# Optimization experiments

Measured on AMD Instinct MI355X. Metric: run time of the kernel, lower is better.

The kernel has to match this reference:

```python
import jax, jax.numpy as jnp
import numpy as np

N_GRAPHS = 64  # number of graphs pooled by global_mean_pool


def setup_inputs() -> dict:
    key = jax.random.key(0)
    ks = jax.random.split(key, 10)
    N, E, H, K = 50000, 800000, 128, 3
    x = jax.random.normal(ks[0], (N, H), dtype=jnp.float32)
    edge_index = jax.random.randint(ks[1], (2, E), 0, N)
    edge_weight = jax.random.uniform(ks[2], (E,), dtype=jnp.float32)
    batch = jnp.sort(jax.random.randint(ks[3], (N,), 0, N_GRAPHS))
    # 5 TAGConv layers, each with K+1 = 4 weight matrices [H,H] and one bias [H]
    conv_ws = jax.random.normal(ks[4], (5, K + 1, H, H), dtype=jnp.float32) * 0.05
    conv_bs = jax.random.normal(ks[5], (5, H), dtype=jnp.float32) * 0.01
    lin1_w = jax.random.normal(ks[6], (H, H), dtype=jnp.float32) * 0.05
    lin1_b = jnp.zeros((H,), dtype=jnp.float32)
    lin2_w = jax.random.normal(ks[7], (H, 1), dtype=jnp.float32) * 0.05
    lin2_b = jnp.zeros((1,), dtype=jnp.float32)
    return {"x": x, "edge_index": edge_index, "edge_weight": edge_weight,
            "batch": batch, "conv_ws": conv_ws, "conv_bs": conv_bs,
            "lin1_w": lin1_w, "lin1_b": lin1_b, "lin2_w": lin2_w, "lin2_b": lin2_b}


def _gcn_norm(edge_index, edge_weight, n):
    # TAGConv default: gcn_norm without self-loops
    row, col = edge_index[0], edge_index[1]
    deg = jax.ops.segment_sum(edge_weight, col, num_segments=n)
    deg_safe = jnp.where(deg > 0, deg, 1.0)
    dis = jnp.where(deg > 0, jax.lax.rsqrt(deg_safe), 0.0)
    return dis[row] * edge_weight * dis[col]


def _tagconv(x, w, b, row, col, norm, n):
    # out = sum_k (A_hat^k x) W_k + b
    out = x @ w[0]
    h = x
    for k in range(1, w.shape[0]):
        h = jax.ops.segment_sum(h[row] * norm[:, None], col, num_segments=n)
        out = out + h @ w[k]
    return out + b


def reference(x, edge_index, edge_weight, batch, conv_ws, conv_bs,
              lin1_w, lin1_b, lin2_w, lin2_b):
    n = x.shape[0]
    row, col = edge_index[0], edge_index[1]
    norm = _gcn_norm(edge_index, edge_weight, n)
    h = x
    for i in range(5):
        h = jax.nn.relu(_tagconv(h, conv_ws[i], conv_bs[i], row, col, norm, n))
    # global mean pool per graph (dropout treated as identity / eval mode)
    sums = jax.ops.segment_sum(h, batch, num_segments=N_GRAPHS)
    cnt = jax.ops.segment_sum(jnp.ones((n,), h.dtype), batch, num_segments=N_GRAPHS)
    g = sums / jnp.maximum(cnt, 1.0)[:, None]
    g = g @ lin1_w + lin1_b
    g = g @ lin2_w + lin2_b
    return jax.nn.sigmoid(g)
```

## Files before the change

kernel.cpp:

```cpp
#include <hip/hip_runtime.h>
#include <math.h>

#define H 128
#define NGRAPH 64

using f32x4 = __attribute__((ext_vector_type(4))) float;
using f32x2 = __attribute__((ext_vector_type(2))) float;

__device__ inline float bf2f(ushort u) {
  unsigned int b = ((unsigned int)u) << 16;
  return __builtin_bit_cast(float, b);
}
__device__ inline ushort f2bf(float f) {
  unsigned int u = __builtin_bit_cast(unsigned int, f);
  u = (u + 0x7FFF + ((u >> 16) & 1)) >> 16;
  return (ushort)u;
}

#define ACC8(accv, v, n)                                                                     \
  {                                                                                          \
    f32x2 c;                                                                                 \
    c = __builtin_amdgcn_cvt_pk_f32_fp8((v).x, false);                                       \
    accv[0] = fmaf(n, c[0], accv[0]); accv[1] = fmaf(n, c[1], accv[1]);                      \
    c = __builtin_amdgcn_cvt_pk_f32_fp8((v).x, true);                                        \
    accv[2] = fmaf(n, c[0], accv[2]); accv[3] = fmaf(n, c[1], accv[3]);                      \
    c = __builtin_amdgcn_cvt_pk_f32_fp8((v).y, false);                                       \
    accv[4] = fmaf(n, c[0], accv[4]); accv[5] = fmaf(n, c[1], accv[5]);                      \
    c = __builtin_amdgcn_cvt_pk_f32_fp8((v).y, true);                                        \
    accv[6] = fmaf(n, c[0], accv[6]); accv[7] = fmaf(n, c[1], accv[7]);                      \
  }

__global__ __launch_bounds__(256) void k_cvt_x(const float* __restrict__ x,
                                               unsigned char* __restrict__ x8, int total4) {
  int i = blockIdx.x * blockDim.x + threadIdx.x;
  if (i >= total4) return;
  float4 v = *(const float4*)(x + (size_t)i * 4);
  int p = __builtin_amdgcn_cvt_pk_fp8_f32(v.x, v.y, 0, false);
  p = __builtin_amdgcn_cvt_pk_fp8_f32(v.z, v.w, p, true);
  *(unsigned int*)(x8 + (size_t)i * 4) = (unsigned int)p;
}

__global__ __launch_bounds__(256) void k_cvt_w(const float* __restrict__ w,
                                               unsigned char* __restrict__ w8, int total4) {
  int i = blockIdx.x * blockDim.x + threadIdx.x;
  if (i >= total4) return;
  int f = i * 4;
  int l = f >> 16;
  int j = (f >> 9) & 127;
  int k = f & 511;
  int q = k >> 7, kk = k & 127;
  const float* src = w + (((size_t)(l * 4 + q) * H + kk) * H + j);
  float v0 = src[0], v1 = src[H], v2 = src[2 * H], v3 = src[3 * H];
  int p = __builtin_amdgcn_cvt_pk_fp8_f32(v0, v1, 0, false);
  p = __builtin_amdgcn_cvt_pk_fp8_f32(v2, v3, p, true);
  *(unsigned int*)(w8 + f) = (unsigned int)p;
}

__global__ void k_count(const int* __restrict__ col, int* __restrict__ cnt,
                        int* __restrict__ rank, int E) {
  int e = blockIdx.x * blockDim.x + threadIdx.x;
  if (e < E) rank[e] = atomicAdd(&cnt[col[e]], 1);
}

__global__ __launch_bounds__(256) void k_scan1(const int* __restrict__ cnt,
                                               int* __restrict__ bsum, int N) {
  int i = blockIdx.x * 256 + threadIdx.x;
  int v = (i < N) ? cnt[i] : 0;
  __shared__ int red[256];
  red[threadIdx.x] = v;
  __syncthreads();
  #pragma unroll
  for (int o = 128; o; o >>= 1) {
    if (threadIdx.x < o) red[threadIdx.x] += red[threadIdx.x + o];
    __syncthreads();
  }
  if (threadIdx.x == 0) bsum[blockIdx.x] = red[0];
}

__global__ __launch_bounds__(256) void k_scan2(const int* __restrict__ bsum,
                                               int* __restrict__ boff, int nb) {
  __shared__ int s[256];
  int t = threadIdx.x;
  int v = (t < nb) ? bsum[t] : 0;
  s[t] = v;
  __syncthreads();
  #pragma unroll
  for (int d = 1; d < 256; d <<= 1) {
    int u = (t >= d) ? s[t - d] : 0;
    __syncthreads();
    s[t] += u;
    __syncthreads();
  }
  if (t < nb) boff[t] = s[t] - v;
}

__global__ __launch_bounds__(256) void k_scan3(const int* __restrict__ cnt,
                                               const int* __restrict__ boff,
                                               int* __restrict__ ptr, int N) {
  int t = threadIdx.x;
  int i = blockIdx.x * 256 + t;
  int v = (i < N) ? cnt[i] : 0;
  __shared__ int s[256];
  s[t] = v;
  __syncthreads();
  #pragma unroll
  for (int d = 1; d < 256; d <<= 1) {
    int u = (t >= d) ? s[t - d] : 0;
    __syncthreads();
    s[t] += u;
    __syncthreads();
  }
  int ex = boff[blockIdx.x] + s[t] - v;
  if (i < N) {
    ptr[i] = ex;
    if (i == N - 1) ptr[N] = ex + v;
  }
}

__global__ void k_scatter(const int* __restrict__ row, const int* __restrict__ col,
                          const float* __restrict__ w, const int* __restrict__ ptr,
                          const int* __restrict__ rank, unsigned int* __restrict__ es, int E) {
  int e = blockIdx.x * blockDim.x + threadIdx.x;
  if (e < E) {
    int pos = ptr[col[e]] + rank[e];
    es[pos] = ((unsigned int)row[e] & 0xFFFFu) | ((unsigned int)f2bf(w[e]) << 16);
  }
}

__global__ __launch_bounds__(256) void k_degnorm1(const int* __restrict__ ptr,
                                                  const unsigned int* __restrict__ es,
                                                  float* __restrict__ dis, int N) {
  int v = blockIdx.x * blockDim.x + threadIdx.x;
  if (v >= N) return;
  int s = ptr[v], e = ptr[v + 1];
  float d = 0.f;
  for (int i = s; i < e; i++) d += bf2f((ushort)(es[i] >> 16));
  dis[v] = d > 0.f ? rsqrtf(d) : 0.f;
}

__global__ __launch_bounds__(256) void k_degnorm2(const int* __restrict__ ptr,
                                                  unsigned int* __restrict__ es,
                                                  const float* __restrict__ dis, int N) {
  int v = blockIdx.x * blockDim.x + threadIdx.x;
  if (v >= N) return;
  int s = ptr[v], e = ptr[v + 1];
  float dv = dis[v];
  for (int i = s; i < e; i++) {
    unsigned int u = es[i];
    float nm = dis[u & 0xFFFFu] * bf2f((ushort)(u >> 16)) * dv;
    es[i] = (u & 0xFFFFu) | ((unsigned int)f2bf(nm) << 16);
  }
}

__global__ __launch_bounds__(256) void k_prop(const unsigned char* __restrict__ hin8,
                                              unsigned char* __restrict__ hout8,
                                              const int* __restrict__ ptr,
                                              const unsigned int* __restrict__ es, int N) {
  int node = (blockIdx.x * 256 + threadIdx.x) >> 4;
  if (node >= N) return;
  int l15 = threadIdx.x & 15;
  int s = ptr[node], e = ptr[node + 1];
  float a[8] = {0.f, 0.f, 0.f, 0.f, 0.f, 0.f, 0.f, 0.f};
  float b[8] = {0.f, 0.f, 0.f, 0.f, 0.f, 0.f, 0.f, 0.f};
  const unsigned char* base = hin8 + l15 * 8;
  int i = s;
  for (; i + 3 < e; i += 4) {
    unsigned int u0 = es[i], u1 = es[i + 1], u2 = es[i + 2], u3 = es[i + 3];
    uint2 v0 = *(const uint2*)(base + (size_t)(u0 & 0xFFFFu) * H);
    uint2 v1 = *(const uint2*)(base + (size_t)(u1 & 0xFFFFu) * H);
    uint2 v2 = *(const uint2*)(base + (size_t)(u2 & 0xFFFFu) * H);
    uint2 v3 = *(const uint2*)(base + (size_t)(u3 & 0xFFFFu) * H);
    float n0 = bf2f((ushort)(u0 >> 16));
    float n1 = bf2f((ushort)(u1 >> 16));
    float n2 = bf2f((ushort)(u2 >> 16));
    float n3 = bf2f((ushort)(u3 >> 16));
    ACC8(a, v0, n0);
    ACC8(b, v1, n1);
    ACC8(a, v2, n2);
    ACC8(b, v3, n3);
  }
  for (; i < e; i++) {
    unsigned int u0 = es[i];
    uint2 v0 = *(const uint2*)(base + (size_t)(u0 & 0xFFFFu) * H);
    float n0 = bf2f((ushort)(u0 >> 16));
    ACC8(a, v0, n0);
  }
  #pragma unroll
  for (int j = 0; j < 8; j++) a[j] += b[j];
  int p0 = __builtin_amdgcn_cvt_pk_fp8_f32(a[0], a[1], 0, false);
  p0 = __builtin_amdgcn_cvt_pk_fp8_f32(a[2], a[3], p0, true);
  int p1 = __builtin_amdgcn_cvt_pk_fp8_f32(a[4], a[5], 0, false);
  p1 = __builtin_amdgcn_cvt_pk_fp8_f32(a[6], a[7], p1, true);
  *(uint2*)(hout8 + (size_t)node * H + l15 * 8) = make_uint2((unsigned int)p0, (unsigned int)p1);
}

__global__ __launch_bounds__(256) void k_fgemm(const unsigned char* __restrict__ X0,
                                               const unsigned char* __restrict__ X1,
                                               const unsigned char* __restrict__ X2,
                                               const unsigned char* __restrict__ X3,
                                               const unsigned char* __restrict__ W8,
                                               const float* __restrict__ bias,
                                               unsigned char* __restrict__ O8, int N) {
  __shared__ unsigned char As[128][72];
  __shared__ unsigned char Bs[128][72];
  int t = threadIdx.x;
  int r0 = blockIdx.x * 128;
  int w = t >> 6, lane = t & 63;
  int mw = w >> 1, nw = w & 1;
  int l15 = lane & 15, l4 = lane >> 4;

  f32x4 acc[4][4];
  #pragma unroll
  for (int i = 0; i < 4; i++)
    #pragma unroll
    for (int j = 0; j < 4; j++) acc[i][j] = (f32x4){0.f, 0.f, 0.f, 0.f};

  for (int it = 0; it < 8; ++it) {
    const unsigned char* Xp = (it < 2) ? X0 : (it < 4) ? X1 : (it < 6) ? X2 : X3;
    int kb = (it & 1) * 64;
    int k0 = it * 64;
    #pragma unroll
    for (int p = 0; p < 2; p++) {
      int idx = t + p * 256;
      int rj = idx >> 2;
      int kc = (idx & 3) << 4;
      int gr = r0 + rj;
      uint4 av = make_uint4(0, 0, 0, 0);
      if (gr < N) av = *(const uint4*)(Xp + (size_t)gr * H + kb + kc);
      *(uint4*)&As[rj][kc] = av;
      *(uint4*)&Bs[rj][kc] = *(const uint4*)(W8 + (size_t)rj * 512 + k0 + kc);
    }
    __syncthreads();
    #pragma unroll
    for (int ks = 0; ks < 2; ks++) {
      int kk = ks * 32 + l4 * 8;
      long a[4], b[4];
      #pragma unroll
      for (int mf = 0; mf < 4; mf++) a[mf] = *(const long*)&As[mw * 64 + mf * 16 + l15][kk];
      #pragma unroll
      for (int nf = 0; nf < 4; nf++) b[nf] = *(const long*)&Bs[nw * 64 + nf * 16 + l15][kk];
      #pragma unroll
      for (int mf = 0; mf < 4; mf++)
        #pragma unroll
        for (int nf = 0; nf < 4; nf++)
          acc[mf][nf] = __builtin_amdgcn_mfma_f32_16x16x32_fp8_fp8(a[mf], b[nf], acc[mf][nf], 0, 0, 0);
    }
    __syncthreads();
  }

  #pragma unroll
  for (int nf = 0; nf < 4; nf++) {
    int colj = nw * 64 + nf * 16 + l15;
    float bv = bias[colj];
    #pragma unroll
    for (int mf = 0; mf < 4; mf++) {
      int rbase = r0 + mw * 64 + mf * 16 + l4 * 4;
      #pragma unroll
      for (int r = 0; r < 4; r++) {
        int rr = rbase + r;
        if (rr < N) {
          float v = fmaxf(acc[mf][nf][r] + bv, 0.f);
          O8[(size_t)rr * H + colj] =
              (unsigned char)(__builtin_amdgcn_cvt_pk_fp8_f32(v, v, 0, false) & 0xFF);
        }
      }
    }
  }
}

#define POOL_ROWS 64
__global__ __launch_bounds__(256) void k_pool(const unsigned char* __restrict__ h8,
                                              const int* __restrict__ batch,
                                              float* __restrict__ pooled, int N) {
  int r0 = blockIdx.x * POOL_ROWS;
  int j2 = threadIdx.x & 63;
  int q = threadIdx.x >> 6;
  int rend = min(r0 + POOL_ROWS, N);
  float a0 = 0.f, a1 = 0.f;
  int cur = -1;
  for (int r = r0 + q; r < rend; r += 4) {
    int g = batch[r];
    if (g != cur) {
      if (cur >= 0) {
        atomicAdd(&pooled[cur * H + 2 * j2], a0);
        atomicAdd(&pooled[cur * H + 2 * j2 + 1], a1);
      }
      cur = g;
      a0 = a1 = 0.f;
    }
    unsigned int v = *(const ushort*)(h8 + (size_t)r * H + 2 * j2);
    f32x2 c = __builtin_amdgcn_cvt_pk_f32_fp8(v, false);
    a0 += c[0];
    a1 += c[1];
  }
  if (cur >= 0) {
    atomicAdd(&pooled[cur * H + 2 * j2], a0);
    atomicAdd(&pooled[cur * H + 2 * j2 + 1], a1);
  }
}

__global__ __launch_bounds__(128) void k_head(const float* __restrict__ pooled,
                                              const int* __restrict__ batch, int N,
                                              const float* __restrict__ w1,
                                              const float* __restrict__ b1,
                                              const float* __restrict__ w2,
                                              const float* __restrict__ b2,
                                              float* __restrict__ out) {
  int g = blockIdx.x;
  int j = threadIdx.x;
  __shared__ float pv[H];
  __shared__ float red[H];
  __shared__ int bnd[2];
  if (j < 2) {
    int target = g + j;
    int lo = 0, hi = N;
    while (lo < hi) {
      int mid = (lo + hi) >> 1;
      if (batch[mid] < target) lo = mid + 1;
      else hi = mid;
    }
    bnd[j] = lo;
  }
  __syncthreads();
  float c = (float)max(bnd[1] - bnd[0], 1);
  pv[j] = pooled[g * H + j] / c;
  __syncthreads();
  float t1 = b1[j];
  #pragma unroll 4
  for (int k = 0; k < H; k++) t1 = fmaf(pv[k], w1[k * H + j], t1);
  red[j] = t1 * w2[j];
  __syncthreads();
  if (j < 64) {
    float s = red[j] + red[j + 64];
    #pragma unroll
    for (int o = 32; o; o >>= 1) s += __shfl_down(s, o);
    if (j == 0) out[g] = 1.f / (1.f + expf(-(s + b2[0])));
  }
}

extern "C" void kernel_launch(void* const* d_in, const int* in_sizes, int n_in,
                              void* d_out, int out_size, void* d_ws, size_t ws_size,
                              hipStream_t stream) {
  const float* x = (const float*)d_in[0];
  const int* eidx = (const int*)d_in[1];
  const float* ew = (const float*)d_in[2];
  const int* batch = (const int*)d_in[3];
  const float* conv_ws = (const float*)d_in[4];
  const float* conv_bs = (const float*)d_in[5];
  const float* lin1_w = (const float*)d_in[6];
  const float* lin1_b = (const float*)d_in[7];
  const float* lin2_w = (const float*)d_in[8];
  const float* lin2_b = (const float*)d_in[9];
  float* out = (float*)d_out;

  const int N = in_sizes[0] / H;
  const int E = in_sizes[2];
  const int* row = eidx;
  const int* col = eidx + E;

  char* p = (char*)d_ws;
  auto alloc = [&](size_t bytes) {
    char* q = p;
    p += (bytes + 255) & ~(size_t)255;
    return q;
  };
  int* cnt = (int*)alloc((size_t)N * 4);
  int* ptrb = (int*)alloc((size_t)(N + 1) * 4);
  int* rank = (int*)alloc((size_t)E * 4);
  float* dis = (float*)alloc((size_t)N * 4);
  unsigned int* es = (unsigned int*)alloc((size_t)E * 4);
  unsigned char* x8 = (unsigned char*)alloc((size_t)N * H);
  unsigned char* C0 = (unsigned char*)alloc((size_t)N * H);
  unsigned char* C1 = (unsigned char*)alloc((size_t)N * H);
  unsigned char* C2 = (unsigned char*)alloc((size_t)N * H);
  unsigned char* C3 = (unsigned char*)alloc((size_t)N * H);
  unsigned char* W8 = (unsigned char*)alloc((size_t)5 * H * 512);
  int* bsum = (int*)alloc(256 * 4);
  int* boff = (int*)alloc(256 * 4);
  float* pooled = (float*)alloc((size_t)NGRAPH * H * 4);

  hipMemsetAsync(cnt, 0, (size_t)N * 4, stream);
  hipMemsetAsync(pooled, 0, (size_t)NGRAPH * H * 4, stream);

  int eb = (E + 255) / 256;
  int nb = (N + 255) / 256;
  k_cvt_x<<<(N * H / 4 + 255) / 256, 256, 0, stream>>>(x, x8, N * H / 4);
  k_cvt_w<<<(5 * H * 512 / 4 + 255) / 256, 256, 0, stream>>>(conv_ws, W8, 5 * H * 512 / 4);
  k_count<<<eb, 256, 0, stream>>>(col, cnt, rank, E);
  k_scan1<<<nb, 256, 0, stream>>>(cnt, bsum, N);
  k_scan2<<<1, 256, 0, stream>>>(bsum, boff, nb);
  k_scan3<<<nb, 256, 0, stream>>>(cnt, boff, ptrb, N);
  k_scatter<<<eb, 256, 0, stream>>>(row, col, ew, ptrb, rank, es, E);
  k_degnorm1<<<nb, 256, 0, stream>>>(ptrb, es, dis, N);
  k_degnorm2<<<nb, 256, 0, stream>>>(ptrb, es, dis, N);

  int gemm_blocks = (N + 127) / 128;
  int prop_blocks = (N + 15) / 16;

  const unsigned char* P8 = x8;
  for (int layer = 0; layer < 5; layer++) {
    const unsigned char* Wl = W8 + (size_t)layer * H * 512;
    const float* bl = conv_bs + (size_t)layer * H;
    k_prop<<<prop_blocks, 256, 0, stream>>>(P8, C0, ptrb, es, N);
    k_prop<<<prop_blocks, 256, 0, stream>>>(C0, C1, ptrb, es, N);
    k_prop<<<prop_blocks, 256, 0, stream>>>(C1, C2, ptrb, es, N);
    k_fgemm<<<gemm_blocks, 256, 0, stream>>>(P8, C0, C1, C2, Wl, bl, C3, N);
    P8 = C3;
  }

  k_pool<<<(N + POOL_ROWS - 1) / POOL_ROWS, 256, 0, stream>>>(P8, batch, pooled, N);
  k_head<<<NGRAPH, 128, 0, stream>>>(pooled, batch, N, lin1_w, lin1_b, lin2_w, lin2_b, out);
}
```

Measured before the change: 481.1 us.

## Split fp8 feature matrices into two 64-column halves and fuse setup kernels

Stores every fp8 node-feature buffer as two planes of 64 columns each, so each propagation pass gathers 64-byte rows and runs as two half-feature sweeps. Each sweep's gather working set (3.2MB) is more likely to stay in cache. The GEMM, pool and conversion kernels are rewritten to use the split layout. Separately, the x conversion, weight conversion and edge-count kernels are merged into one launch to cut launch overhead. The cost is that edge lists are read twice per propagation and there are twice as many prop blocks.

Measured after the change: 507.9 us. 1.06x slower.

```diff
diff --git a/kernel.cpp b/kernel.cpp
--- a/kernel.cpp
+++ b/kernel.cpp
@@ -30,36 +30,44 @@
     accv[6] = fmaf(n, c[0], accv[6]); accv[7] = fmaf(n, c[1], accv[7]);                      \
   }
 
-__global__ __launch_bounds__(256) void k_cvt_x(const float* __restrict__ x,
-                                               unsigned char* __restrict__ x8, int total4) {
-  int i = blockIdx.x * blockDim.x + threadIdx.x;
-  if (i >= total4) return;
-  float4 v = *(const float4*)(x + (size_t)i * 4);
-  int p = __builtin_amdgcn_cvt_pk_fp8_f32(v.x, v.y, 0, false);
-  p = __builtin_amdgcn_cvt_pk_fp8_f32(v.z, v.w, p, true);
-  *(unsigned int*)(x8 + (size_t)i * 4) = (unsigned int)p;
-}
-
-__global__ __launch_bounds__(256) void k_cvt_w(const float* __restrict__ w,
-                                               unsigned char* __restrict__ w8, int total4) {
-  int i = blockIdx.x * blockDim.x + threadIdx.x;
-  if (i >= total4) return;
-  int f = i * 4;
-  int l = f >> 16;
-  int j = (f >> 9) & 127;
-  int k = f & 511;
-  int q = k >> 7, kk = k & 127;
-  const float* src = w + (((size_t)(l * 4 + q) * H + kk) * H + j);
-  float v0 = src[0], v1 = src[H], v2 = src[2 * H], v3 = src[3 * H];
-  int p = __builtin_amdgcn_cvt_pk_fp8_f32(v0, v1, 0, false);
-  p = __builtin_amdgcn_cvt_pk_fp8_f32(v2, v3, p, true);
-  *(unsigned int*)(w8 + f) = (unsigned int)p;
-}
-
-__global__ void k_count(const int* __restrict__ col, int* __restrict__ cnt,
-                        int* __restrict__ rank, int E) {
-  int e = blockIdx.x * blockDim.x + threadIdx.x;
-  if (e < E) rank[e] = atomicAdd(&cnt[col[e]], 1);
+__global__ __launch_bounds__(256) void k_setup(const float* __restrict__ x,
+                                               unsigned char* __restrict__ x8,
+                                               const float* __restrict__ w,
+                                               unsigned char* __restrict__ w8,
+                                               const int* __restrict__ col,
+                                               int* __restrict__ cnt, int* __restrict__ rank,
+                                               int nx4, int nw4, int E, int bx, int bw,
+                                               size_t N64) {
+  int b = blockIdx.x;
+  int t = threadIdx.x;
+  if (b < bx) {
+    int i = b * 256 + t;
+    if (i < nx4) {
+      float4 v = *(const float4*)(x + (size_t)i * 4);
+      int p = __builtin_amdgcn_cvt_pk_fp8_f32(v.x, v.y, 0, false);
+      p = __builtin_amdgcn_cvt_pk_fp8_f32(v.z, v.w, p, true);
+      int f = i * 4;
+      int r = f >> 7, c = f & 127;
+      *(unsigned int*)(x8 + (size_t)(c >> 6) * N64 + (size_t)r * 64 + (c & 63)) = (unsigned int)p;
+    }
+  } else if (b < bx + bw) {
+    int i = (b - bx) * 256 + t;
+    if (i < nw4) {
+      int f = i * 4;
+      int l = f >> 16;
+      int j = (f >> 9) & 127;
+      int k = f & 511;
+      int q = k >> 7, kk = k & 127;
+      const float* src = w + (((size_t)(l * 4 + q) * H + kk) * H + j);
+      float v0 = src[0], v1 = src[H], v2 = src[2 * H], v3 = src[3 * H];
+      int p = __builtin_amdgcn_cvt_pk_fp8_f32(v0, v1, 0, false);
+      p = __builtin_amdgcn_cvt_pk_fp8_f32(v2, v3, p, true);
+      *(unsigned int*)(w8 + f) = (unsigned int)p;
+    }
+  } else {
+    int e = (b - bx - bw) * 256 + t;
+    if (e < E) rank[e] = atomicAdd(&cnt[col[e]], 1);
+  }
 }
 
 __global__ __launch_bounds__(256) void k_scan1(const int* __restrict__ cnt,
@@ -155,43 +163,48 @@
 __global__ __launch_bounds__(256) void k_prop(const unsigned char* __restrict__ hin8,
                                               unsigned char* __restrict__ hout8,
                                               const int* __restrict__ ptr,
-                                              const unsigned int* __restrict__ es, int N) {
-  int node = (blockIdx.x * 256 + threadIdx.x) >> 4;
+                                              const unsigned int* __restrict__ es,
+                                              int N, int nbh, size_t N64) {
+  int b = blockIdx.x;
+  size_t off = 0;
+  if (b >= nbh) { b -= nbh; off = N64; }
+  int node = b * 32 + (threadIdx.x >> 3);
   if (node >= N) return;
-  int l15 = threadIdx.x & 15;
+  int l7 = threadIdx.x & 7;
   int s = ptr[node], e = ptr[node + 1];
   float a[8] = {0.f, 0.f, 0.f, 0.f, 0.f, 0.f, 0.f, 0.f};
-  float b[8] = {0.f, 0.f, 0.f, 0.f, 0.f, 0.f, 0.f, 0.f};
-  const unsigned char* base = hin8 + l15 * 8;
+  float bb[8] = {0.f, 0.f, 0.f, 0.f, 0.f, 0.f, 0.f, 0.f};
+  const unsigned char* base = hin8 + off + l7 * 8;
   int i = s;
   for (; i + 3 < e; i += 4) {
     unsigned int u0 = es[i], u1 = es[i + 1], u2 = es[i + 2], u3 = es[i + 3];
-    uint2 v0 = *(const uint2*)(base + (size_t)(u0 & 0xFFFFu) * H);
-    uint2 v1 = *(const uint2*)(base + (size_t)(u1 & 0xFFFFu) * H);
-    uint2 v2 = *(const uint2*)(base + (size_t)(u2 & 0xFFFFu) * H);
-    uint2 v3 = *(const uint2*)(base + (size_t)(u3 & 0xFFFFu) * H);
+    uint2 v0 = *(const uint2*)(base + (size_t)(u0 & 0xFFFFu) * 64);
+    uint2 v1 = *(const uint2*)(base + (size_t)(u1 & 0xFFFFu) * 64);
+    uint2 v2 = *(const uint2*)(base + (size_t)(u2 & 0xFFFFu) * 64);
+    uint2 v3 = *(const uint2*)(base + (size_t)(u3 & 0xFFFFu) * 64);
     float n0 = bf2f((ushort)(u0 >> 16));
     float n1 = bf2f((ushort)(u1 >> 16));
     float n2 = bf2f((ushort)(u2 >> 16));
     float n3 = bf2f((ushort)(u3 >> 16));
     ACC8(a, v0, n0);
-    ACC8(b, v1, n1);
+    ACC8(bb, v1, n1);
     ACC8(a, v2, n2);
-    ACC8(b, v3, n3);
+    ACC8(bb, v3, n3);
   }
   for (; i < e; i++) {
     unsigned int u0 = es[i];
-    uint2 v0 = *(const uint2*)(base + (size_t)(u0 & 0xFFFFu) * H);
+    uint2 v0 = *(const uint2*)(base + (size_t)(u0 & 0xFFFFu) * 64);
     float n0 = bf2f((ushort)(u0 >> 16));
     ACC8(a, v0, n0);
   }
   #pragma unroll
-  for (int j = 0; j < 8; j++) a[j] += b[j];
+  for (int j = 0; j < 8; j++) a[j] += bb[j];
   int p0 = __builtin_amdgcn_cvt_pk_fp8_f32(a[0], a[1], 0, false);
   p0 = __builtin_amdgcn_cvt_pk_fp8_f32(a[2], a[3], p0, true);
   int p1 = __builtin_amdgcn_cvt_pk_fp8_f32(a[4], a[5], 0, false);
   p1 = __builtin_amdgcn_cvt_pk_fp8_f32(a[6], a[7], p1, true);
-  *(uint2*)(hout8 + (size_t)node * H + l15 * 8) = make_uint2((unsigned int)p0, (unsigned int)p1);
+  *(uint2*)(hout8 + off + (size_t)node * 64 + l7 * 8) =
+      make_uint2((unsigned int)p0, (unsigned int)p1);
 }
 
 __global__ __launch_bounds__(256) void k_fgemm(const unsigned char* __restrict__ X0,
@@ -200,7 +213,8 @@
                                                const unsigned char* __restrict__ X3,
                                                const unsigned char* __restrict__ W8,
                                                const float* __restrict__ bias,
-                                               unsigned char* __restrict__ O8, int N) {
+                                               unsigned char* __restrict__ O8, int N,
+                                               size_t N64) {
   __shared__ unsigned char As[128][72];
   __shared__ unsigned char Bs[128][72];
   int t = threadIdx.x;
@@ -217,7 +231,7 @@
 
   for (int it = 0; it < 8; ++it) {
     const unsigned char* Xp = (it < 2) ? X0 : (it < 4) ? X1 : (it < 6) ? X2 : X3;
-    int kb = (it & 1) * 64;
+    const unsigned char* Xs = Xp + (size_t)(it & 1) * N64;
     int k0 = it * 64;
     #pragma unroll
     for (int p = 0; p < 2; p++) {
@@ -226,7 +240,7 @@
       int kc = (idx & 3) << 4;
       int gr = r0 + rj;
       uint4 av = make_uint4(0, 0, 0, 0);
-      if (gr < N) av = *(const uint4*)(Xp + (size_t)gr * H + kb + kc);
+      if (gr < N) av = *(const uint4*)(Xs + (size_t)gr * 64 + kc);
       *(uint4*)&As[rj][kc] = av;
       *(uint4*)&Bs[rj][kc] = *(const uint4*)(W8 + (size_t)rj * 512 + k0 + kc);
     }
@@ -251,6 +265,7 @@
   #pragma unroll
   for (int nf = 0; nf < 4; nf++) {
     int colj = nw * 64 + nf * 16 + l15;
+    unsigned char* Od = O8 + (size_t)(colj >> 6) * N64 + (colj & 63);
     float bv = bias[colj];
     #pragma unroll
     for (int mf = 0; mf < 4; mf++) {
@@ -260,7 +275,7 @@
         int rr = rbase + r;
         if (rr < N) {
           float v = fmaxf(acc[mf][nf][r] + bv, 0.f);
-          O8[(size_t)rr * H + colj] =
+          Od[(size_t)rr * 64] =
               (unsigned char)(__builtin_amdgcn_cvt_pk_fp8_f32(v, v, 0, false) & 0xFF);
         }
       }
@@ -271,10 +286,12 @@
 #define POOL_ROWS 64
 __global__ __launch_bounds__(256) void k_pool(const unsigned char* __restrict__ h8,
                                               const int* __restrict__ batch,
-                                              float* __restrict__ pooled, int N) {
+                                              float* __restrict__ pooled, int N, size_t N64) {
   int r0 = blockIdx.x * POOL_ROWS;
   int j2 = threadIdx.x & 63;
   int q = threadIdx.x >> 6;
+  int c = 2 * j2;
+  const unsigned char* hb = h8 + (size_t)(c >> 6) * N64 + (c & 63);
   int rend = min(r0 + POOL_ROWS, N);
   float a0 = 0.f, a1 = 0.f;
   int cur = -1;
@@ -282,20 +299,20 @@
     int g = batch[r];
     if (g != cur) {
       if (cur >= 0) {
-        atomicAdd(&pooled[cur * H + 2 * j2], a0);
-        atomicAdd(&pooled[cur * H + 2 * j2 + 1], a1);
+        atomicAdd(&pooled[cur * H + c], a0);
+        atomicAdd(&pooled[cur * H + c + 1], a1);
       }
       cur = g;
       a0 = a1 = 0.f;
     }
-    unsigned int v = *(const ushort*)(h8 + (size_t)r * H + 2 * j2);
-    f32x2 c = __builtin_amdgcn_cvt_pk_f32_fp8(v, false);
-    a0 += c[0];
-    a1 += c[1];
+    unsigned int v = *(const ushort*)(hb + (size_t)r * 64);
+    f32x2 cc = __builtin_amdgcn_cvt_pk_f32_fp8(v, false);
+    a0 += cc[0];
+    a1 += cc[1];
   }
   if (cur >= 0) {
-    atomicAdd(&pooled[cur * H + 2 * j2], a0);
-    atomicAdd(&pooled[cur * H + 2 * j2 + 1], a1);
+    atomicAdd(&pooled[cur * H + c], a0);
+    atomicAdd(&pooled[cur * H + c + 1], a1);
   }
 }
 
@@ -357,6 +374,7 @@
   const int E = in_sizes[2];
   const int* row = eidx;
   const int* col = eidx + E;
+  const size_t N64 = (size_t)N * 64;
 
   char* p = (char*)d_ws;
   auto alloc = [&](size_t bytes) {
@@ -382,32 +400,36 @@
   hipMemsetAsync(cnt, 0, (size_t)N * 4, stream);
   hipMemsetAsync(pooled, 0, (size_t)NGRAPH * H * 4, stream);
 
-  int eb = (E + 255) / 256;
+  int nx4 = N * H / 4;
+  int nw4 = 5 * H * 512 / 4;
+  int bx = (nx4 + 255) / 256;
+  int bw = (nw4 + 255) / 256;
+  int be = (E + 255) / 256;
   int nb = (N + 255) / 256;
-  k_cvt_x<<<(N * H / 4 + 255) / 256, 256, 0, stream>>>(x, x8, N * H / 4);
-  k_cvt_w<<<(5 * H * 512 / 4 + 255) / 256, 256, 0, stream>>>(conv_ws, W8, 5 * H * 512 / 4);
-  k_count<<<eb, 256, 0, stream>>>(col, cnt, rank, E);
+  k_setup<<<bx + bw + be, 256, 0, stream>>>(x, x8, conv_ws, W8, col, cnt, rank,
+                                            nx4, nw4, E, bx, bw, N64);
   k_scan1<<<nb, 256, 0, stream>>>(cnt, bsum, N);
   k_scan2<<<1, 256, 0, stream>>>(bsum, boff, nb);
   k_scan3<<<nb, 256, 0, stream>>>(cnt, boff, ptrb, N);
-  k_scatter<<<eb, 256, 0, stream>>>(row, col, ew, ptrb, rank, es, E);
+  k_scatter<<<be, 256, 0, stream>>>(row, col, ew, ptrb, rank, es, E);
   k_degnorm1<<<nb, 256, 0, stream>>>(ptrb, es, dis, N);
   k_degnorm2<<<nb, 256, 0, stream>>>(ptrb, es, dis, N);
 
   int gemm_blocks = (N + 127) / 128;
-  int prop_blocks = (N + 15) / 16;
+  int nbh = (N + 31) / 32;
+  int prop_blocks = 2 * nbh;
 
   const unsigned char* P8 = x8;
   for (int layer = 0; layer < 5; layer++) {
     const unsigned char* Wl = W8 + (size_t)layer * H * 512;
     const float* bl = conv_bs + (size_t)layer * H;
-    k_prop<<<prop_blocks, 256, 0, stream>>>(P8, C0, ptrb, es, N);
-    k_prop<<<prop_blocks, 256, 0, stream>>>(C0, C1, ptrb, es, N);
-    k_prop<<<prop_blocks, 256, 0, stream>>>(C1, C2, ptrb, es, N);
-    k_fgemm<<<gemm_blocks, 256, 0, stream>>>(P8, C0, C1, C2, Wl, bl, C3, N);
+    k_prop<<<prop_blocks, 256, 0, stream>>>(P8, C0, ptrb, es, N, nbh, N64);
+    k_prop<<<prop_blocks, 256, 0, stream>>>(C0, C1, ptrb, es, N, nbh, N64);
+    k_prop<<<prop_blocks, 256, 0, stream>>>(C1, C2, ptrb, es, N, nbh, N64);
+    k_fgemm<<<gemm_blocks, 256, 0, stream>>>(P8, C0, C1, C2, Wl, bl, C3, N, N64);
     P8 = C3;
   }
 
-  k_pool<<<(N + POOL_ROWS - 1) / POOL_ROWS, 256, 0, stream>>>(P8, batch, pooled, N);
+  k_pool<<<(N + POOL_ROWS - 1) / POOL_ROWS, 256, 0, stream>>>(P8, batch, pooled, N, N64);
   k_head<<<NGRAPH, 128, 0, stream>>>(pooled, batch, N, lin1_w, lin1_b, lin2_w, lin2_b, out);
 }
```
